# Kernel optimization log

Hardware: AMD Instinct MI355X
Metric: run time of the kernel (lower is better)

Reference implementation:

```python
import jax, jax.numpy as jnp
import numpy as np

CUTOFF = 1.5   # cutoff_val from __init__
M = 48         # atoms per molecule (batch_node_vec is block-structured: node n belongs to molecule n // M)
B = 128        # number of molecules


def setup_inputs() -> dict:
    key = jax.random.key(0)
    k1, k2 = jax.random.split(key)
    N = B * M
    coords = jax.random.normal(k1, (N, 3), dtype=jnp.float32)
    atomic_ns = jax.random.randint(k2, (N,), 0, 10)
    batch_node_vec = jnp.arange(N, dtype=jnp.int64) // M
    return {"atomic_ns": atomic_ns, "coords": coords, "batch_node_vec": batch_node_vec}


def _forward(coords):
    # coords: [N, 3]; molecules are contiguous blocks of M atoms -> dense per-molecule blocks.
    N = coords.shape[0]
    c = coords.reshape(N // M, M, 3)                      # [B, M, 3]
    diff = c[:, :, None, :] - c[:, None, :, :]            # diff[b,p,q] = r_p - r_q, [B,M,M,3]
    d2 = jnp.sum(diff * diff, axis=-1)                    # squared pair distances [B,M,M]
    offdiag = ~jnp.eye(M, dtype=bool)
    dist = jnp.sqrt(jnp.where(offdiag, d2, 1.0))          # safe sqrt (diagonal masked out)
    adj = offdiag & (dist < CUTOFF)                       # radius graph within each molecule
    dists = jnp.where(adj, dist, 0.0)                     # per-edge distances (masked dense form)

    # Triplets k->j->i (DimeNet): angle at center j between (r_i - r_j) and (r_k - r_j), i != k.
    v = jnp.swapaxes(diff, 1, 2)                          # v[b,j,i] = r_i - r_j, [B,M,M,3]
    a = jnp.einsum('bjid,bjkd->bjik', v, v)               # dot products [B,M,M,M]
    n2 = d2                                               # |v[b,j,i]|^2 (d2 is symmetric)
    # |u x w|^2 = |u|^2 |w|^2 - (u.w)^2  (same value as torch.cross(...).norm()**2)
    b2 = jnp.maximum(n2[:, :, :, None] * n2[:, :, None, :] - a * a, 0.0)
    tmask = adj[:, :, :, None] & adj[:, :, None, :] & offdiag[None, None, :, :]  # edges (j,i),(j,k), i!=k
    b_safe = jnp.sqrt(jnp.where(tmask & (b2 > 0), b2, 1.0))
    b_val = jnp.where(b2 > 0, b_safe, 0.0)
    a_safe = jnp.where(tmask, a, 1.0)
    ang = jnp.arctan2(b_val, a_safe)
    angles = jnp.where(tmask, ang, 0.0)                   # [B,M,M,M] masked triplet angles
    return dists, angles


def reference(atomic_ns, coords, batch_node_vec):
    # atomic_ns / batch_node_vec only determine graph structure (ints); geometry uses coords.
    return _forward(coords)
```

## Files before the change

kernel.cpp:

```cpp
#include <hip/hip_runtime.h>

#define MM 48
#define BMOL 128
#define CUTOFF_V 1.5f

__global__ __launch_bounds__(256)
void dimenet_dist_angle_kernel(const float* __restrict__ coords,
                               float* __restrict__ dists,
                               float* __restrict__ angles)
{
    const int bj = blockIdx.x;
    const int b  = bj / MM;
    const int j  = bj - b * MM;

    __shared__ float vx[MM], vy[MM], vz[MM], n2s[MM];
    __shared__ int   adjs[MM];

    const int tid = threadIdx.x;

    if (tid < MM) {
        const float* cj = coords + 3 * ((size_t)b * MM + j);
        const float* ci = coords + 3 * ((size_t)b * MM + tid);
        float dx = ci[0] - cj[0];
        float dy = ci[1] - cj[1];
        float dz = ci[2] - cj[2];
        float d2 = dx * dx + dy * dy + dz * dz;
        float dist = sqrtf(d2);
        bool adj = (tid != j) && (dist < CUTOFF_V);
        vx[tid] = dx;
        vy[tid] = dy;
        vz[tid] = dz;
        n2s[tid] = d2;
        adjs[tid] = adj ? 1 : 0;
        dists[((size_t)b * MM + j) * MM + tid] = adj ? dist : 0.0f;
    }
    __syncthreads();

    float* ang_base = angles + ((size_t)b * MM + j) * MM * MM;

    for (int idx = tid; idx < MM * MM; idx += 256) {
        int i = idx / MM;
        int k = idx - i * MM;
        bool tm = adjs[i] && adjs[k] && (i != k);
        float ang = 0.0f;
        if (tm) {
            float a  = vx[i] * vx[k] + vy[i] * vy[k] + vz[i] * vz[k];
            float b2 = fmaxf(n2s[i] * n2s[k] - a * a, 0.0f);
            float bv = (b2 > 0.0f) ? sqrtf(b2) : 0.0f;
            ang = atan2f(bv, a);
        }
        ang_base[idx] = ang;
    }
}

extern "C" void kernel_launch(void* const* d_in, const int* in_sizes, int n_in,
                              void* d_out, int out_size, void* d_ws, size_t ws_size,
                              hipStream_t stream) {
    const float* coords = (const float*)d_in[1];

    float* out    = (float*)d_out;
    float* dists  = out;
    float* angles = out + (size_t)BMOL * MM * MM;

    dim3 grid(BMOL * MM);
    dim3 block(256);
    dimenet_dist_angle_kernel<<<grid, block, 0, stream>>>(coords, dists, angles);
}
```

Measured before the change: 22.28 us.

## Replace atan2 with polynomial acos and vectorize angle stores with one float4 per thread

Angles are computed as acos of the normalized dot product using a fast polynomial approximation instead of atan2f of cross and dot magnitudes. Each of 576 threads computes four consecutive outputs and writes them with a single float4 store, removing the strided loop. The adjacency mask is folded into a per-atom inverse-norm weight. This trades exactness for fewer instructions and risks a larger numerical error than the atan2 version.

```diff
diff --git a/kernel.cpp b/kernel.cpp
--- a/kernel.cpp
+++ b/kernel.cpp
@@ -3,8 +3,9 @@
 #define MM 48
 #define BMOL 128
 #define CUTOFF_V 1.5f
+#define PI_F 3.14159265358979f
 
-__global__ __launch_bounds__(256)
+__global__ __launch_bounds__(576)
 void dimenet_dist_angle_kernel(const float* __restrict__ coords,
                                float* __restrict__ dists,
                                float* __restrict__ angles)
@@ -13,44 +14,61 @@
     const int b  = bj / MM;
     const int j  = bj - b * MM;
 
-    __shared__ float vx[MM], vy[MM], vz[MM], n2s[MM];
-    __shared__ int   adjs[MM];
+    __shared__ __align__(16) float sx[MM];
+    __shared__ __align__(16) float sy[MM];
+    __shared__ __align__(16) float sz[MM];
+    __shared__ __align__(16) float sw[MM];
 
-    const int tid = threadIdx.x;
+    const int t = threadIdx.x;
 
-    if (tid < MM) {
+    if (t < MM) {
         const float* cj = coords + 3 * ((size_t)b * MM + j);
-        const float* ci = coords + 3 * ((size_t)b * MM + tid);
+        const float* ci = coords + 3 * ((size_t)b * MM + t);
         float dx = ci[0] - cj[0];
         float dy = ci[1] - cj[1];
         float dz = ci[2] - cj[2];
         float d2 = dx * dx + dy * dy + dz * dz;
         float dist = sqrtf(d2);
-        bool adj = (tid != j) && (dist < CUTOFF_V);
-        vx[tid] = dx;
-        vy[tid] = dy;
-        vz[tid] = dz;
-        n2s[tid] = d2;
-        adjs[tid] = adj ? 1 : 0;
-        dists[((size_t)b * MM + j) * MM + tid] = adj ? dist : 0.0f;
+        bool adj = (t != j) && (dist < CUTOFF_V);
+        sx[t] = dx;
+        sy[t] = dy;
+        sz[t] = dz;
+        sw[t] = adj ? rsqrtf(d2) : 0.0f;
+        dists[((size_t)b * MM + j) * MM + t] = adj ? dist : 0.0f;
     }
     __syncthreads();
 
-    float* ang_base = angles + ((size_t)b * MM + j) * MM * MM;
+    const int i  = t / 12;
+    const int k0 = (t - i * 12) * 4;
 
-    for (int idx = tid; idx < MM * MM; idx += 256) {
-        int i = idx / MM;
-        int k = idx - i * MM;
-        bool tm = adjs[i] && adjs[k] && (i != k);
-        float ang = 0.0f;
-        if (tm) {
-            float a  = vx[i] * vx[k] + vy[i] * vy[k] + vz[i] * vz[k];
-            float b2 = fmaxf(n2s[i] * n2s[k] - a * a, 0.0f);
-            float bv = (b2 > 0.0f) ? sqrtf(b2) : 0.0f;
-            ang = atan2f(bv, a);
-        }
-        ang_base[idx] = ang;
+    const float xi = sx[i], yi = sy[i], zi = sz[i], wi = sw[i];
+    const float4 xk = *(const float4*)&sx[k0];
+    const float4 yk = *(const float4*)&sy[k0];
+    const float4 zk = *(const float4*)&sz[k0];
+    const float4 wk = *(const float4*)&sw[k0];
+
+    const float* pxk = &xk.x;
+    const float* pyk = &yk.x;
+    const float* pzk = &zk.x;
+    const float* pwk = &wk.x;
+
+    float ang[4];
+#pragma unroll
+    for (int e = 0; e < 4; ++e) {
+        float a = xi * pxk[e] + yi * pyk[e] + zi * pzk[e];
+        float w = wi * pwk[e];
+        float x = a * w;
+        x = fminf(fmaxf(x, -1.0f), 1.0f);
+        float s = fabsf(x);
+        float p = sqrtf(1.0f - s) *
+                  (1.5707288f + s * (-0.2121144f + s * (0.074261f - 0.0187293f * s)));
+        float r = (x >= 0.0f) ? p : (PI_F - p);
+        bool mask = (w > 0.0f) && (i != k0 + e);
+        ang[e] = mask ? r : 0.0f;
     }
+
+    float4 res = make_float4(ang[0], ang[1], ang[2], ang[3]);
+    *(float4*)(angles + (((size_t)b * MM + j) * MM + i) * MM + k0) = res;
 }
 
 extern "C" void kernel_launch(void* const* d_in, const int* in_sizes, int n_in,
@@ -63,6 +81,6 @@
     float* angles = out + (size_t)BMOL * MM * MM;
 
     dim3 grid(BMOL * MM);
-    dim3 block(256);
+    dim3 block(576);
     dimenet_dist_angle_kernel<<<grid, block, 0, stream>>>(coords, dists, angles);
 }
```

Result: faster. 21.42 us (-3.9%).
